# Performance work log

Hardware: AMD Instinct MI355X
Metric: run time of the kernel (lower is better)

## Reference

```python
import jax, jax.numpy as jnp
import numpy as np
from jax import lax

BIG = 1e8  # sentinel 'infinity'; safe in fp32 since max (i-j)^2 ~ 512^2


def _dt1d(f, axis):
    """Exact 1-D squared-distance transform along `axis`:
    d[i] = min_j (i-j)^2 + f[j]. Scanned over j (min-plus), fully vectorized
    over all other dims."""
    f = jnp.moveaxis(f, axis, -1)
    shp = f.shape
    n = shp[-1]
    fr = f.reshape(-1, n)  # [R, n]
    idx = jnp.arange(n, dtype=f.dtype)

    def step(d, xs):
        fj, j = xs  # fj: [R], j: scalar position
        cand = fj[:, None] + (idx - j) ** 2  # [R, n]
        return jnp.minimum(d, cand), None

    d0 = jnp.full_like(fr, BIG)
    d, _ = lax.scan(step, d0, (fr.T, idx))
    return jnp.moveaxis(d.reshape(shp), -1, axis)


def _edt(mask):
    """Exact Euclidean distance transform: distance from every element to the
    nearest True element of `mask` (0 where mask is True). Matches
    scipy.ndimage.distance_transform_edt(~mask applied as in the torch module)
    via the exact separable squared-distance decomposition, over ALL dims
    (including batch/channel, as the original code does)."""
    f = jnp.where(mask, 0.0, BIG).astype(jnp.float32)
    for ax in range(f.ndim):
        f = _dt1d(f, ax)
    return jnp.sqrt(f)


def setup_inputs() -> dict:
    key = jax.random.key(0)
    k1, k2 = jax.random.split(key)
    shape = (8, 1, 512, 512)
    x = jax.random.normal(k1, shape, dtype=jnp.float32)
    # sparse binary label mask (~1/64 foreground) for non-trivial distances
    y = (jax.random.randint(k2, shape, 0, 64) == 0).astype(jnp.int32)
    return {"x": x, "y": y}


def reference(x, y):
    # original: dist = EDT(logical_not(y)) = distance to nearest nonzero of y
    d = _edt(y != 0)
    return (jax.nn.sigmoid(x) * d).mean()
```

## Files before the change

### kernel.cpp

```cpp
#include <hip/hip_runtime.h>
#include <math.h>

#define BIGV 1.0e8f
#define PLANE (512 * 512)
#define NTOT  (8 * PLANE)
#define NSPATIAL PLANE

__global__ __launch_bounds__(512) void dt_axis3(const int* __restrict__ y,
                                                float* __restrict__ g1) {
    __shared__ unsigned long long words[8];
    int i = threadIdx.x;
    int e = blockIdx.x * 512 + i;
    int set = (y[e] != 0) ? 1 : 0;
    unsigned long long bal = __ballot(set);
    int wid  = i >> 6;
    int lane = i & 63;
    if (lane == 0) words[wid] = bal;
    __syncthreads();

    int k = wid, b = lane;
    int dr = 1 << 30;
    {
        unsigned long long m0 = words[k] & (~0ull << b);
        if (m0) {
            dr = (__ffsll((long long)m0) - 1) - b;
        } else {
            #pragma unroll
            for (int k2 = 0; k2 < 8; ++k2) {
                if (k2 > k && dr == (1 << 30) && words[k2]) {
                    dr = (k2 << 6) + (__ffsll((long long)words[k2]) - 1) - i;
                }
            }
        }
    }
    int dl = 1 << 30;
    {
        unsigned long long m0 = words[k] & (~0ull >> (63 - b));
        if (m0) {
            dl = b - (63 - __clzll((long long)m0));
        } else {
            #pragma unroll
            for (int k2 = 7; k2 >= 0; --k2) {
                if (k2 < k && dl == (1 << 30) && words[k2]) {
                    dl = i - ((k2 << 6) + 63 - __clzll((long long)words[k2]));
                }
            }
        }
    }
    int d = min(dl, dr);
    g1[e] = (d > 511) ? BIGV : (float)(d * d);
}

__global__ __launch_bounds__(256) void dt_axis2(const float* __restrict__ g1,
                                                float* __restrict__ g2) {
    int e = blockIdx.x * 256 + threadIdx.x;
    int b   = e >> 18;
    int rem = e & (PLANE - 1);
    int i2  = rem >> 9;
    int i3  = rem & 511;
    const float* col = g1 + b * PLANE + i3;
    float m = col[i2 << 9];
    for (int r = 1; r < 512; ++r) {
        float r2 = (float)(r * r);
        if (r2 >= m) break;
        int lo = i2 - r, hi = i2 + r;
        if (lo >= 0)  m = fminf(m, col[lo << 9] + r2);
        if (hi < 512) m = fminf(m, col[hi << 9] + r2);
        if (lo < 0 && hi >= 512) break;
    }
    g2[e] = m;
}

__device__ inline double wave_reduce_d(double v) {
    #pragma unroll
    for (int off = 32; off > 0; off >>= 1) v += __shfl_down(v, off, 64);
    return v;
}

__global__ __launch_bounds__(256) void axis0_epilogue(const float* __restrict__ g2,
                                                      const float* __restrict__ x,
                                                      double* __restrict__ partials) {
    int s = blockIdx.x * 256 + threadIdx.x;
    float v[8];
    #pragma unroll
    for (int b = 0; b < 8; ++b) v[b] = g2[b * PLANE + s];

    double acc = 0.0;
    #pragma unroll
    for (int b = 0; b < 8; ++b) {
        float m = BIGV;
        #pragma unroll
        for (int bp = 0; bp < 8; ++bp) {
            float db = (float)((b - bp) * (b - bp));
            m = fminf(m, v[bp] + db);
        }
        float xv  = x[b * PLANE + s];
        float sig = 1.0f / (1.0f + expf(-xv));
        acc += (double)(sig * sqrtf(m));
    }

    __shared__ double lds[4];
    double w = wave_reduce_d(acc);
    int lane = threadIdx.x & 63;
    int wid  = threadIdx.x >> 6;
    if (lane == 0) lds[wid] = w;
    __syncthreads();
    if (wid == 0) {
        double t = (lane < 4) ? lds[lane] : 0.0;
        #pragma unroll
        for (int off = 2; off > 0; off >>= 1) t += __shfl_down(t, off, 64);
        if (lane == 0) partials[blockIdx.x] = t;
    }
}

__global__ __launch_bounds__(256) void finalize(const double* __restrict__ partials,
                                                float* __restrict__ out) {
    double a = 0.0;
    for (int i = threadIdx.x; i < 1024; i += 256) a += partials[i];
    __shared__ double lds[4];
    double w = wave_reduce_d(a);
    int lane = threadIdx.x & 63;
    int wid  = threadIdx.x >> 6;
    if (lane == 0) lds[wid] = w;
    __syncthreads();
    if (threadIdx.x == 0) {
        double total = lds[0] + lds[1] + lds[2] + lds[3];
        out[0] = (float)(total / (double)NTOT);
    }
}

extern "C" void kernel_launch(void* const* d_in, const int* in_sizes, int n_in,
                              void* d_out, int out_size, void* d_ws, size_t ws_size,
                              hipStream_t stream) {
    const float* x = (const float*)d_in[0];
    const int*   y = (const int*)d_in[1];
    float* out = (float*)d_out;

    float*  g1       = (float*)d_ws;
    float*  g2       = g1 + NTOT;
    double* partials = (double*)(g2 + NTOT);

    dt_axis3<<<NTOT / 512, 512, 0, stream>>>(y, g1);
    dt_axis2<<<NTOT / 256, 256, 0, stream>>>(g1, g2);
    axis0_epilogue<<<NSPATIAL / 256, 256, 0, stream>>>(g2, x, partials);
    finalize<<<1, 256, 0, stream>>>(partials, out);
}
```

Measured before the change: 105.0 us.

## Fuse column transform into axis0 epilogue and store row distances as ushort

The row-distance intermediate is now stored as 16-bit unsigned distances instead of fp32 squared distances, halving its footprint and read traffic. The column (axis 2) transform is fused into the batch-axis epilogue kernel, so the g2 buffer write and read plus one kernel launch are gone. The cost is that each thread now runs eight serial column scans, one per batch, with only PLANE/256 blocks launched. That cuts parallelism eightfold and may expose memory latency.

```diff
diff --git a/kernel.cpp b/kernel.cpp
--- a/kernel.cpp
+++ b/kernel.cpp
@@ -4,10 +4,10 @@
 #define BIGV 1.0e8f
 #define PLANE (512 * 512)
 #define NTOT  (8 * PLANE)
-#define NSPATIAL PLANE
+#define DINF  0x7FFF
 
 __global__ __launch_bounds__(512) void dt_axis3(const int* __restrict__ y,
-                                                float* __restrict__ g1) {
+                                                unsigned short* __restrict__ g1) {
     __shared__ unsigned long long words[8];
     int i = threadIdx.x;
     int e = blockIdx.x * 512 + i;
@@ -48,27 +48,11 @@
         }
     }
     int d = min(dl, dr);
-    g1[e] = (d > 511) ? BIGV : (float)(d * d);
+    g1[e] = (d > 511) ? (unsigned short)DINF : (unsigned short)d;
 }
 
-__global__ __launch_bounds__(256) void dt_axis2(const float* __restrict__ g1,
-                                                float* __restrict__ g2) {
-    int e = blockIdx.x * 256 + threadIdx.x;
-    int b   = e >> 18;
-    int rem = e & (PLANE - 1);
-    int i2  = rem >> 9;
-    int i3  = rem & 511;
-    const float* col = g1 + b * PLANE + i3;
-    float m = col[i2 << 9];
-    for (int r = 1; r < 512; ++r) {
-        float r2 = (float)(r * r);
-        if (r2 >= m) break;
-        int lo = i2 - r, hi = i2 + r;
-        if (lo >= 0)  m = fminf(m, col[lo << 9] + r2);
-        if (hi < 512) m = fminf(m, col[hi << 9] + r2);
-        if (lo < 0 && hi >= 512) break;
-    }
-    g2[e] = m;
+__device__ inline float conv_g1(unsigned short u) {
+    return (u == DINF) ? BIGV : (float)((int)u * (int)u);
 }
 
 __device__ inline double wave_reduce_d(double v) {
@@ -77,13 +61,29 @@
     return v;
 }
 
-__global__ __launch_bounds__(256) void axis0_epilogue(const float* __restrict__ g2,
-                                                      const float* __restrict__ x,
-                                                      double* __restrict__ partials) {
-    int s = blockIdx.x * 256 + threadIdx.x;
+__global__ __launch_bounds__(256) void dt2_axis0_epilogue(
+        const unsigned short* __restrict__ g1,
+        const float* __restrict__ x,
+        double* __restrict__ partials) {
+    int s  = blockIdx.x * 256 + threadIdx.x;
+    int i2 = s >> 9;
+    int i3 = s & 511;
+
     float v[8];
     #pragma unroll
-    for (int b = 0; b < 8; ++b) v[b] = g2[b * PLANE + s];
+    for (int b = 0; b < 8; ++b) {
+        const unsigned short* col = g1 + b * PLANE + i3;
+        float m = conv_g1(col[i2 << 9]);
+        for (int r = 1; r < 512; ++r) {
+            float r2 = (float)(r * r);
+            if (r2 >= m) break;
+            int lo = i2 - r, hi = i2 + r;
+            if (lo >= 0)  m = fminf(m, conv_g1(col[lo << 9]) + r2);
+            if (hi < 512) m = fminf(m, conv_g1(col[hi << 9]) + r2);
+            if (lo < 0 && hi >= 512) break;
+        }
+        v[b] = m;
+    }
 
     double acc = 0.0;
     #pragma unroll
@@ -136,12 +136,10 @@
     const int*   y = (const int*)d_in[1];
     float* out = (float*)d_out;
 
-    float*  g1       = (float*)d_ws;
-    float*  g2       = g1 + NTOT;
-    double* partials = (double*)(g2 + NTOT);
+    unsigned short* g1 = (unsigned short*)d_ws;
+    double* partials   = (double*)((char*)d_ws + NTOT * sizeof(unsigned short));
 
     dt_axis3<<<NTOT / 512, 512, 0, stream>>>(y, g1);
-    dt_axis2<<<NTOT / 256, 256, 0, stream>>>(g1, g2);
-    axis0_epilogue<<<NSPATIAL / 256, 256, 0, stream>>>(g2, x, partials);
+    dt2_axis0_epilogue<<<PLANE / 256, 256, 0, stream>>>(g1, x, partials);
     finalize<<<1, 256, 0, stream>>>(partials, out);
 }
```

Measured after the change: 119.0 us. +13.3%, slower.
